# Kernel optimization log

Measured on AMD Instinct MI355X. Metric: run time of the kernel, lower is better.

Reference implementation:

```python
import jax, jax.numpy as jnp
import numpy as np

B, N1, N2, D = 32, 1024, 1024, 128
OUT = 64            # fc1 output / pooled width
SCALE = 0.5         # (input_size // output_size) ** -0.5 = 4 ** -0.5
EPS = 1e-12         # torch F.normalize eps


def _l2norm(x):
    n = jnp.linalg.norm(x, axis=-1, keepdims=True)
    return x / jnp.maximum(n, EPS)


def setup_inputs() -> dict:
    key = jax.random.key(0)
    k1, k2, k3, k4 = jax.random.split(key, 4)
    drug_1 = jax.random.normal(k1, (B, N1, D), dtype=jnp.float32)
    drug_2 = jax.random.normal(k2, (B, N2, D), dtype=jnp.float32)
    # fc1: Linear(256 -> 64), torch default init ~ U(-1/sqrt(256), 1/sqrt(256))
    bound = 1.0 / np.sqrt(2 * D)
    fc1_w = jax.random.uniform(k3, (OUT, 2 * D), jnp.float32, -bound, bound)
    fc1_b = jax.random.uniform(k4, (OUT,), jnp.float32, -bound, bound)
    return {"drug_1": drug_1, "drug_2": drug_2, "fc1_w": fc1_w, "fc1_b": fc1_b}


def reference(drug_1, drug_2, fc1_w, fc1_b):
    d1 = _l2norm(drug_1)                                   # [B,N1,D]
    d2 = _l2norm(drug_2)                                   # [B,N2,D]
    aff = jnp.einsum("bnd,bmd->bnm", d1, d2) * SCALE       # [B,N1,N2]
    s1 = jax.nn.softmax(aff, axis=-1)                      # softmax over N2
    s2 = jax.nn.softmax(aff, axis=-2)                      # softmax over N1
    drug1_layer = jnp.einsum("bnm,bnd->bmd", s2, d1)       # [B,N2,D]
    drug2_layer = jnp.einsum("bnm,bmd->bnd", s1, d2)       # [B,N1,D]
    drug1_emb = jnp.concatenate([d1, drug2_layer], axis=-1)   # [B,N1,2D]
    drug2_emb = jnp.concatenate([d2, drug1_layer], axis=-1)   # [B,N2,2D]
    fusion = jnp.concatenate([drug1_emb, drug2_emb], axis=1)  # [B,N1+N2,2D]
    # dropout treated as identity (deterministic reference)
    w = jax.nn.relu(jnp.einsum("bnf,of->bno", fusion, fc1_w) + fc1_b)
    w = jax.nn.softmax(w, axis=-1)                          # [B,N1+N2,OUT]
    pooled = fusion.reshape(fusion.shape[:-1] + (OUT, 4)).mean(-1)  # AvgPool1d(4)
    return pooled * w
```

## Files before the change

### kernel.cpp

```cpp
#include <hip/hip_runtime.h>

#define Bz   32
#define Nn   1024
#define Dd   128
#define OUTW 64
#define CEXP 0.72134752044448169f
#define LOG2E 1.4426950408889634f

typedef __attribute__((ext_vector_type(8))) short bf16x8;
typedef __attribute__((ext_vector_type(4))) short bf16x4;
typedef __attribute__((ext_vector_type(4))) float f32x4;

static __device__ __forceinline__ unsigned short f2bf(float x) {
    unsigned u = __float_as_uint(x);
    u += 0x7FFFu + ((u >> 16) & 1u);
    return (unsigned short)(u >> 16);
}
static __device__ __forceinline__ float bf2f(short b) {
    return __uint_as_float(((unsigned)(unsigned short)b) << 16);
}
static __device__ __forceinline__ unsigned cvt_pk_bf16(float lo, float hi) {
    unsigned r;
    asm("v_cvt_pk_bf16_f32 %0, %1, %2" : "=v"(r) : "v"(lo), "v"(hi));
    return r;
}
#define GLL16(g, l) __builtin_amdgcn_global_load_lds( \
    (const __attribute__((address_space(1))) unsigned*)(const void*)(g), \
    (__attribute__((address_space(3))) unsigned*)(void*)(l), 16, 0, 0)
#define WAITVN(n) { asm volatile("s_waitcnt vmcnt(" #n ")" ::: "memory"); \
                    __builtin_amdgcn_sched_barrier(0); }
#define SBAR() __builtin_amdgcn_s_barrier()


__global__ __launch_bounds__(256) void k_norm(const float* __restrict__ drug1,
                                              const float* __restrict__ drug2,
                                              short* __restrict__ d1s,
                                              short* __restrict__ d2s,
                                              short* __restrict__ d1ts,
                                              short* __restrict__ d2ts) {
    __shared__ __attribute__((aligned(16))) short T[Dd * 64];
    const int tid = threadIdx.x, wave = tid >> 6, lane = tid & 63;
    const int b = blockIdx.y;
    const int n0 = blockIdx.x * 64;
    const float* src; short* dstR; short* dstT;
    if (blockIdx.z == 0) { src = drug1; dstR = d1s; dstT = d1ts; }
    else                 { src = drug2; dstR = d2s; dstT = d2ts; }

    const int rh = lane >> 5;
    const int c  = lane & 31;
    #pragma unroll
    for (int i = 0; i < 8; ++i) {
        const int col = wave * 16 + i * 2 + rh;
        const int n = n0 + col;
        const float4 v = *(const float4*)(src + ((long)b * Nn + n) * Dd + c * 4);
        float ss = v.x * v.x + v.y * v.y + v.z * v.z + v.w * v.w;
        #pragma unroll
        for (int msk = 1; msk < 32; msk <<= 1) ss += __shfl_xor(ss, msk, 64);
        const float inv = 1.0f / fmaxf(sqrtf(ss), 1e-12f);
        const unsigned p0 = cvt_pk_bf16(v.x * inv, v.y * inv);
        const unsigned p1 = cvt_pk_bf16(v.z * inv, v.w * inv);
        uint2 u2; u2.x = p0; u2.y = p1;
        *(uint2*)(dstR + ((long)b * Nn + n) * Dd + ((c * 4) ^ ((n & 7) * 8))) = u2;
        const unsigned short e0 = (unsigned short)(p0 & 0xFFFF);
        const unsigned short e1 = (unsigned short)(p0 >> 16);
        const unsigned short e2 = (unsigned short)(p1 & 0xFFFF);
        const unsigned short e3 = (unsigned short)(p1 >> 16);
        const int Csw = (16 * (c >> 3)) ^ (8 * (c & 3));
        const int pc = col ^ Csw;
        T[(c * 4 + 0) * 64 + pc] = (short)e0;
        T[(c * 4 + 1) * 64 + pc] = (short)e1;
        T[(c * 4 + 2) * 64 + pc] = (short)e2;
        T[(c * 4 + 3) * 64 + pc] = (short)e3;
    }
    __syncthreads();
    const int d = tid >> 1, h = tid & 1;
    const int C = (16 * (d >> 5)) ^ (8 * ((d >> 2) & 3));
    short* wtp = dstT + ((long)b * Dd + d) * Nn + n0;
    #pragma unroll
    for (int k = 0; k < 4; ++k) {
        const int gi = h * 4 + k;
        *(bf16x8*)(wtp + ((gi ^ (d & 7)) * 8)) =
            *(const bf16x8*)&T[d * 64 + ((gi * 8) ^ C)];
    }
}

__global__ __launch_bounds__(256, 2) void k_attn(const short* __restrict__ d1s,
                                                 const short* __restrict__ d2s,
                                                 const short* __restrict__ d1ts,
                                                 const short* __restrict__ d2ts,
                                                 short* __restrict__ layerA,
                                                 short* __restrict__ layerB) {
    __shared__ __attribute__((aligned(16))) short Kl[2][64][128];
    __shared__ __attribute__((aligned(16))) short Vl[2][128][64];

    const int bid = blockIdx.x;
    const int xcd = bid & 7, tt = bid >> 3;
    const int jq = tt & 7, gq = tt >> 3;
    const int grp = xcd + 8 * gq;
    const int b = grp & 31, z = grp >> 5;

    const int tid = threadIdx.x, wave = tid >> 6, lane = tid & 63;
    const int m = lane & 15, g = lane >> 4;
    const short *Q, *Ks, *Vts; short* O;
    if (z == 0) { Q = d1s; Ks = d2s; Vts = d2ts; O = layerA; }
    else        { Q = d2s; Ks = d1s; Vts = d1ts; O = layerB; }
    const int q0 = jq * 128 + wave * 32;
    const int sw = (m & 7) * 8;

    const short* Qb = Q + ((long)b * Nn + q0) * Dd;
    bf16x8 qf[2][4];
    #pragma unroll
    for (int qt = 0; qt < 2; ++qt)
        #pragma unroll
        for (int c = 0; c < 4; ++c)
            qf[qt][c] = *(const bf16x8*)(Qb + (qt * 16 + m) * Dd
                                            + ((c * 32 + g * 8) ^ sw));

    f32x4 oacc[2][8];
    f32x4 acc_l[2];
    #pragma unroll
    for (int qt = 0; qt < 2; ++qt) {
        acc_l[qt] = (f32x4){0.f, 0.f, 0.f, 0.f};
        #pragma unroll
        for (int t = 0; t < 8; ++t) oacc[qt][t] = (f32x4){0.f, 0.f, 0.f, 0.f};
    }
    bf16x8 ones;
    #pragma unroll
    for (int j = 0; j < 8; ++j) ones[j] = (short)0x3F80;

    const short* Ksb = Ks  + (long)b * Nn * Dd;
    const short* Vtb = Vts + (long)b * Dd * Nn;
    const int klr = lane >> 4, klc = lane & 15;
    const int vlr = lane >> 3, vlc = lane & 7;
    const int srcA = m + 32 * (g & 1);
    const bool glo = (g < 2);

    auto STAGE = [&](int buf, int tile) {
        const int kv0 = tile * 64;
        #pragma unroll
        for (int j = 0; j < 4; ++j)
            GLL16(Ksb + ((long)(kv0 + wave * 16 + j * 4 + klr)) * Dd + klc * 8,
                  &Kl[buf][wave * 16 + j * 4][0]);
        #pragma unroll
        for (int j = 0; j < 4; ++j)
            GLL16(Vtb + ((long)(wave * 32 + j * 8 + vlr)) * Nn + kv0 + vlc * 8,
                  &Vl[buf][wave * 32 + j * 8][0]);
    };

    auto HALF = [&](int buf, int kvsub) {
        f32x4 st[2][2];
        #pragma unroll
        for (int qt = 0; qt < 2; ++qt)
            #pragma unroll
            for (int kt = 0; kt < 2; ++kt) st[qt][kt] = (f32x4){0.f, 0.f, 0.f, 0.f};
        __builtin_amdgcn_s_setprio(1);
        #pragma unroll
        for (int kt = 0; kt < 2; ++kt)
            #pragma unroll
            for (int c = 0; c < 4; ++c) {
                const bf16x8 kf = *(const bf16x8*)
                    &Kl[buf][kvsub + kt * 16 + m][(c * 32 + g * 8) ^ sw];
                st[0][kt] = __builtin_amdgcn_mfma_f32_16x16x32_bf16(kf, qf[0][c], st[0][kt], 0, 0, 0);
                st[1][kt] = __builtin_amdgcn_mfma_f32_16x16x32_bf16(kf, qf[1][c], st[1][kt], 0, 0, 0);
            }
        __builtin_amdgcn_s_setprio(0);
        bf16x8 vf[8];
        #pragma unroll
        for (int t = 0; t < 8; ++t)
            vf[t] = *(const bf16x8*)&Vl[buf][t * 16 + m][(kvsub + g * 8) ^ sw];
        #pragma unroll
        for (int qt = 0; qt < 2; ++qt) {
            unsigned pk[2][2];
            #pragma unroll
            for (int kt = 0; kt < 2; ++kt) {
                const float e0 = exp2f(st[qt][kt][0] * CEXP);
                const float e1 = exp2f(st[qt][kt][1] * CEXP);
                const float e2 = exp2f(st[qt][kt][2] * CEXP);
                const float e3 = exp2f(st[qt][kt][3] * CEXP);
                pk[kt][0] = cvt_pk_bf16(e0, e1);
                pk[kt][1] = cvt_pk_bf16(e2, e3);
            }
            const unsigned w0 = __shfl(pk[0][0], srcA, 64);
            const unsigned w1 = __shfl(pk[0][1], srcA, 64);
            const unsigned w2 = __shfl(pk[0][0], srcA + 16, 64);
            const unsigned w3 = __shfl(pk[0][1], srcA + 16, 64);
            const unsigned x0 = __shfl(pk[1][0], srcA, 64);
            const unsigned x1 = __shfl(pk[1][1], srcA, 64);
            const unsigned x2 = __shfl(pk[1][0], srcA + 16, 64);
            const unsigned x3 = __shfl(pk[1][1], srcA + 16, 64);
            union { unsigned u[4]; bf16x8 v; } af;
            af.u[0] = glo ? w0 : x0;
            af.u[1] = glo ? w1 : x1;
            af.u[2] = glo ? w2 : x2;
            af.u[3] = glo ? w3 : x3;
            __builtin_amdgcn_s_setprio(1);
            #pragma unroll
            for (int t = 0; t < 8; ++t)
                oacc[qt][t] = __builtin_amdgcn_mfma_f32_16x16x32_bf16(af.v, vf[t], oacc[qt][t], 0, 0, 0);
            acc_l[qt] = __builtin_amdgcn_mfma_f32_16x16x32_bf16(af.v, ones, acc_l[qt], 0, 0, 0);
            __builtin_amdgcn_s_setprio(0);
        }
    };

    STAGE(0, 0);
    int cur = 0;
    for (int t = 0; t < 16; ++t) {
        if (t < 15) {
            STAGE(cur ^ 1, t + 1);
            WAITVN(8);
        } else {
            WAITVN(0);
        }
        SBAR();
        HALF(cur, 0);
        HALF(cur, 32);
        asm volatile("s_waitcnt lgkmcnt(0)" ::: "memory");
        SBAR();
        cur ^= 1;
    }

    short* ob = O + ((long)b * Nn + q0) * Dd;
    #pragma unroll
    for (int qt = 0; qt < 2; ++qt)
        #pragma unroll
        for (int r = 0; r < 4; ++r) {
            const float inv = 1.0f / acc_l[qt][r];
            #pragma unroll
            for (int t = 0; t < 8; ++t)
                ob[(qt * 16 + 4 * g + r) * Dd + t * 16 + m] =
                    (short)f2bf(oacc[qt][t][r] * inv);
        }
}

__global__ __launch_bounds__(256, 2) void k_fuse(const float* __restrict__ drug1,
                                                 const float* __restrict__ drug2,
                                                 const short* __restrict__ d1s,
                                                 const short* __restrict__ d2s,
                                                 const short* __restrict__ layA,
                                                 const short* __restrict__ layB,
                                                 const float* __restrict__ fc1w,
                                                 const float* __restrict__ fc1b,
                                                 float* __restrict__ out) {
    const int tid = threadIdx.x, wave = tid >> 6, lane = tid & 63;
    const int m = lane & 15, g = lane >> 4;

    bf16x8 wb[4][8];
    #pragma unroll
    for (int t = 0; t < 4; ++t)
        #pragma unroll
        for (int c = 0; c < 8; ++c) {
            const float* wp = fc1w + (t * 16 + m) * 256 + c * 32 + g * 8;
            const float4 a = *(const float4*)wp;
            const float4 bq = *(const float4*)(wp + 4);
            union { unsigned u[4]; bf16x8 v; } pk;
            pk.u[0] = cvt_pk_bf16(a.x, a.y);
            pk.u[1] = cvt_pk_bf16(a.z, a.w);
            pk.u[2] = cvt_pk_bf16(bq.x, bq.y);
            pk.u[3] = cvt_pk_bf16(bq.z, bq.w);
            wb[t][c] = pk.v;
        }
    float bias[4];
    #pragma unroll
    for (int t = 0; t < 4; ++t) bias[t] = fc1b[t * 16 + m];

    #pragma unroll
    for (int cc = 0; cc < 2; ++cc) {
        const int row0 = blockIdx.x * 128 + cc * 64 + wave * 16;
        const int bb = row0 >> 11;
        const int i0 = row0 & 2047;
        const bool hf = (i0 >= Nn);
        const int ii = hf ? i0 - Nn : i0;
        const short* dsrc = (hf ? d2s : d1s) + ((long)bb * Nn + ii) * Dd;
        const short* lsrc = (hf ? layB : layA) + ((long)bb * Nn + ii) * Dd;
        const float* fsrc = (hf ? drug2 : drug1) + ((long)bb * Nn + ii) * Dd;

        f32x4 acc[4];
        #pragma unroll
        for (int t = 0; t < 4; ++t) acc[t] = (f32x4){0.f, 0.f, 0.f, 0.f};
        #pragma unroll
        for (int c = 0; c < 8; ++c) {
            const short* ap = (c < 4)
                ? dsrc + (long)m * Dd + ((c * 32 + g * 8) ^ ((m & 7) * 8))
                : lsrc + (long)m * Dd + (c - 4) * 32 + g * 8;
            const bf16x8 af = *(const bf16x8*)ap;
            #pragma unroll
            for (int t = 0; t < 4; ++t)
                acc[t] = __builtin_amdgcn_mfma_f32_16x16x32_bf16(af, wb[t][c], acc[t], 0, 0, 0);
        }
        #pragma unroll
        for (int r = 0; r < 4; ++r) {
            float v[4];
            #pragma unroll
            for (int t = 0; t < 4; ++t) v[t] = fmaxf(acc[t][r] + bias[t], 0.f);
            float mx = fmaxf(fmaxf(v[0], v[1]), fmaxf(v[2], v[3]));
            #pragma unroll
            for (int msk = 1; msk < 16; msk <<= 1)
                mx = fmaxf(mx, __shfl_xor(mx, msk, 64));
            float e[4], sum = 0.f;
            #pragma unroll
            for (int t = 0; t < 4; ++t) { e[t] = exp2f((v[t] - mx) * LOG2E); sum += e[t]; }
            #pragma unroll
            for (int msk = 1; msk < 16; msk <<= 1) sum += __shfl_xor(sum, msk, 64);
            const float rinv = 1.0f / sum;

            const int rr = 4 * g + r;
            const float* fr = fsrc + (long)rr * Dd;
            const short* lr = lsrc + (long)rr * Dd;
            const float4 d0 = *(const float4*)(fr + 4 * m);
            const float4 d1 = *(const float4*)(fr + 64 + 4 * m);
            float ss = d0.x*d0.x + d0.y*d0.y + d0.z*d0.z + d0.w*d0.w
                     + d1.x*d1.x + d1.y*d1.y + d1.z*d1.z + d1.w*d1.w;
            #pragma unroll
            for (int msk = 1; msk < 16; msk <<= 1) ss += __shfl_xor(ss, msk, 64);
            const float ninv = 1.0f / fmaxf(sqrtf(ss), 1e-12f);
            const short4 l0 = *(const short4*)(lr + 4 * m);
            const short4 l1 = *(const short4*)(lr + 64 + 4 * m);
            float pooled[4];
            pooled[0] = 0.25f * (d0.x + d0.y + d0.z + d0.w) * ninv;
            pooled[1] = 0.25f * (d1.x + d1.y + d1.z + d1.w) * ninv;
            pooled[2] = 0.25f * (bf2f(l0.x) + bf2f(l0.y) + bf2f(l0.z) + bf2f(l0.w));
            pooled[3] = 0.25f * (bf2f(l1.x) + bf2f(l1.y) + bf2f(l1.z) + bf2f(l1.w));
            float* op = out + ((long)row0 + rr) * OUTW;
            #pragma unroll
            for (int t = 0; t < 4; ++t) op[t * 16 + m] = pooled[t] * (e[t] * rinv);
        }
    }
}

extern "C" void kernel_launch(void* const* d_in, const int* in_sizes, int n_in,
                              void* d_out, int out_size, void* d_ws, size_t ws_size,
                              hipStream_t stream) {
    const float* drug1 = (const float*)d_in[0];
    const float* drug2 = (const float*)d_in[1];
    const float* fc1w  = (const float*)d_in[2];
    const float* fc1b  = (const float*)d_in[3];
    float* out = (float*)d_out;

    char* ws = (char*)d_ws;
    short* d1s    = (short*)(ws);
    short* d2s    = (short*)(ws + 8388608);
    short* d1ts   = (short*)(ws + 16777216);
    short* d2ts   = (short*)(ws + 25165824);
    short* layerA = (short*)(ws + 33554432);
    short* layerB = (short*)(ws + 41943040);

    hipLaunchKernelGGL(k_norm, dim3(16, 32, 2), dim3(256), 0, stream,
                       drug1, drug2, d1s, d2s, d1ts, d2ts);
    hipLaunchKernelGGL(k_attn, dim3(512), dim3(256), 0, stream,
                       d1s, d2s, d1ts, d2ts, layerA, layerB);
    hipLaunchKernelGGL(k_fuse, dim3(512), dim3(256), 0, stream,
                       drug1, drug2, d1s, d2s, layerA, layerB, fc1w, fc1b, out);
}
```

Before: 168.1 us.

## Switch attention to 32x32x16 MFMA with permlane swap and scalar row sums

Rewrites the attention inner loop to use 32x32x16 bf16 MFMA tiles instead of 16x16x32. It builds the P operand in registers with v_permlane32_swap in place of eight cross-lane shuffles, and replaces the ones-vector MFMA row-sum with a plain register accumulation. The fuse kernel also stops rereading the fp32 inputs and recomputing norms, and pools from the already normalized bf16 copies instead. The goal is fewer MFMA and shuffle instructions and less global traffic, at the cost of bf16 precision in the pooled branch and different register pressure.

```diff
diff --git a/kernel.cpp b/kernel.cpp
--- a/kernel.cpp
+++ b/kernel.cpp
@@ -10,6 +10,7 @@
 typedef __attribute__((ext_vector_type(8))) short bf16x8;
 typedef __attribute__((ext_vector_type(4))) short bf16x4;
 typedef __attribute__((ext_vector_type(4))) float f32x4;
+typedef __attribute__((ext_vector_type(16))) float f32x16;
 
 static __device__ __forceinline__ unsigned short f2bf(float x) {
     unsigned u = __float_as_uint(x);
@@ -24,6 +25,8 @@
     asm("v_cvt_pk_bf16_f32 %0, %1, %2" : "=v"(r) : "v"(lo), "v"(hi));
     return r;
 }
+#define PLSWAP(a, b) asm("v_permlane32_swap_b32 %0, %1" : "+v"(a), "+v"(b))
+
 #define GLL16(g, l) __builtin_amdgcn_global_load_lds( \
     (const __attribute__((address_space(1))) unsigned*)(const void*)(g), \
     (__attribute__((address_space(3))) unsigned*)(void*)(l), 16, 0, 0)
@@ -100,40 +103,29 @@
     const int b = grp & 31, z = grp >> 5;
 
     const int tid = threadIdx.x, wave = tid >> 6, lane = tid & 63;
-    const int m = lane & 15, g = lane >> 4;
+    const int r31 = lane & 31, h8 = lane >> 5, r7 = lane & 7;
     const short *Q, *Ks, *Vts; short* O;
     if (z == 0) { Q = d1s; Ks = d2s; Vts = d2ts; O = layerA; }
     else        { Q = d2s; Ks = d1s; Vts = d1ts; O = layerB; }
     const int q0 = jq * 128 + wave * 32;
-    const int sw = (m & 7) * 8;
 
     const short* Qb = Q + ((long)b * Nn + q0) * Dd;
-    bf16x8 qf[2][4];
-    #pragma unroll
-    for (int qt = 0; qt < 2; ++qt)
-        #pragma unroll
-        for (int c = 0; c < 4; ++c)
-            qf[qt][c] = *(const bf16x8*)(Qb + (qt * 16 + m) * Dd
-                                            + ((c * 32 + g * 8) ^ sw));
-
-    f32x4 oacc[2][8];
-    f32x4 acc_l[2];
-    #pragma unroll
-    for (int qt = 0; qt < 2; ++qt) {
-        acc_l[qt] = (f32x4){0.f, 0.f, 0.f, 0.f};
-        #pragma unroll
-        for (int t = 0; t < 8; ++t) oacc[qt][t] = (f32x4){0.f, 0.f, 0.f, 0.f};
-    }
-    bf16x8 ones;
-    #pragma unroll
-    for (int j = 0; j < 8; ++j) ones[j] = (short)0x3F80;
+    bf16x8 qf[8];
+    #pragma unroll
+    for (int c = 0; c < 8; ++c)
+        qf[c] = *(const bf16x8*)(Qb + (long)r31 * Dd + (((2 * c + h8) ^ r7) * 8));
+
+    f32x16 oacc[4];
+    #pragma unroll
+    for (int dblk = 0; dblk < 4; ++dblk)
+        #pragma unroll
+        for (int r = 0; r < 16; ++r) oacc[dblk][r] = 0.f;
+    float lsum = 0.f;
 
     const short* Ksb = Ks  + (long)b * Nn * Dd;
     const short* Vtb = Vts + (long)b * Dd * Nn;
     const int klr = lane >> 4, klc = lane & 15;
     const int vlr = lane >> 3, vlc = lane & 7;
-    const int srcA = m + 32 * (g & 1);
-    const bool glo = (g < 2);
 
     auto STAGE = [&](int buf, int tile) {
         const int kv0 = tile * 64;
@@ -147,59 +139,50 @@
                   &Vl[buf][wave * 32 + j * 8][0]);
     };
 
-    auto HALF = [&](int buf, int kvsub) {
-        f32x4 st[2][2];
-        #pragma unroll
-        for (int qt = 0; qt < 2; ++qt)
-            #pragma unroll
-            for (int kt = 0; kt < 2; ++kt) st[qt][kt] = (f32x4){0.f, 0.f, 0.f, 0.f};
+    auto SUB = [&](int buf, int sub) {
+        f32x16 st;
+        #pragma unroll
+        for (int r = 0; r < 16; ++r) st[r] = 0.f;
         __builtin_amdgcn_s_setprio(1);
         #pragma unroll
-        for (int kt = 0; kt < 2; ++kt)
-            #pragma unroll
-            for (int c = 0; c < 4; ++c) {
-                const bf16x8 kf = *(const bf16x8*)
-                    &Kl[buf][kvsub + kt * 16 + m][(c * 32 + g * 8) ^ sw];
-                st[0][kt] = __builtin_amdgcn_mfma_f32_16x16x32_bf16(kf, qf[0][c], st[0][kt], 0, 0, 0);
-                st[1][kt] = __builtin_amdgcn_mfma_f32_16x16x32_bf16(kf, qf[1][c], st[1][kt], 0, 0, 0);
-            }
+        for (int c = 0; c < 8; ++c) {
+            const bf16x8 kf = *(const bf16x8*)
+                &Kl[buf][sub * 32 + r31][((2 * c + h8) ^ r7) * 8];
+            st = __builtin_amdgcn_mfma_f32_32x32x16_bf16(kf, qf[c], st, 0, 0, 0);
+        }
         __builtin_amdgcn_s_setprio(0);
-        bf16x8 vf[8];
-        #pragma unroll
-        for (int t = 0; t < 8; ++t)
-            vf[t] = *(const bf16x8*)&Vl[buf][t * 16 + m][(kvsub + g * 8) ^ sw];
-        #pragma unroll
-        for (int qt = 0; qt < 2; ++qt) {
-            unsigned pk[2][2];
-            #pragma unroll
-            for (int kt = 0; kt < 2; ++kt) {
-                const float e0 = exp2f(st[qt][kt][0] * CEXP);
-                const float e1 = exp2f(st[qt][kt][1] * CEXP);
-                const float e2 = exp2f(st[qt][kt][2] * CEXP);
-                const float e3 = exp2f(st[qt][kt][3] * CEXP);
-                pk[kt][0] = cvt_pk_bf16(e0, e1);
-                pk[kt][1] = cvt_pk_bf16(e2, e3);
-            }
-            const unsigned w0 = __shfl(pk[0][0], srcA, 64);
-            const unsigned w1 = __shfl(pk[0][1], srcA, 64);
-            const unsigned w2 = __shfl(pk[0][0], srcA + 16, 64);
-            const unsigned w3 = __shfl(pk[0][1], srcA + 16, 64);
-            const unsigned x0 = __shfl(pk[1][0], srcA, 64);
-            const unsigned x1 = __shfl(pk[1][1], srcA, 64);
-            const unsigned x2 = __shfl(pk[1][0], srcA + 16, 64);
-            const unsigned x3 = __shfl(pk[1][1], srcA + 16, 64);
-            union { unsigned u[4]; bf16x8 v; } af;
-            af.u[0] = glo ? w0 : x0;
-            af.u[1] = glo ? w1 : x1;
-            af.u[2] = glo ? w2 : x2;
-            af.u[3] = glo ? w3 : x3;
-            __builtin_amdgcn_s_setprio(1);
-            #pragma unroll
-            for (int t = 0; t < 8; ++t)
-                oacc[qt][t] = __builtin_amdgcn_mfma_f32_16x16x32_bf16(af.v, vf[t], oacc[qt][t], 0, 0, 0);
-            acc_l[qt] = __builtin_amdgcn_mfma_f32_16x16x32_bf16(af.v, ones, acc_l[qt], 0, 0, 0);
-            __builtin_amdgcn_s_setprio(0);
-        }
+        bf16x8 vf[2][4];
+        #pragma unroll
+        for (int kvh = 0; kvh < 2; ++kvh)
+            #pragma unroll
+            for (int dblk = 0; dblk < 4; ++dblk)
+                vf[kvh][dblk] = *(const bf16x8*)
+                    &Vl[buf][dblk * 32 + r31][((4 * sub + 2 * kvh + h8) ^ r7) * 8];
+        float p[16];
+        #pragma unroll
+        for (int r = 0; r < 16; ++r) p[r] = exp2f(st[r] * CEXP);
+        float s4[4];
+        #pragma unroll
+        for (int k = 0; k < 4; ++k)
+            s4[k] = (p[4 * k] + p[4 * k + 1]) + (p[4 * k + 2] + p[4 * k + 3]);
+        lsum += (s4[0] + s4[1]) + (s4[2] + s4[3]);
+        unsigned u0 = cvt_pk_bf16(p[0], p[1]),  u1 = cvt_pk_bf16(p[2], p[3]);
+        unsigned u2 = cvt_pk_bf16(p[4], p[5]),  u3 = cvt_pk_bf16(p[6], p[7]);
+        unsigned u4 = cvt_pk_bf16(p[8], p[9]),  u5 = cvt_pk_bf16(p[10], p[11]);
+        unsigned u6 = cvt_pk_bf16(p[12], p[13]), u7 = cvt_pk_bf16(p[14], p[15]);
+        PLSWAP(u0, u2); PLSWAP(u1, u3);
+        PLSWAP(u4, u6); PLSWAP(u5, u7);
+        union { unsigned u[4]; bf16x8 v; } f0, f1;
+        f0.u[0] = u0; f0.u[1] = u1; f0.u[2] = u2; f0.u[3] = u3;
+        f1.u[0] = u4; f1.u[1] = u5; f1.u[2] = u6; f1.u[3] = u7;
+        __builtin_amdgcn_s_setprio(1);
+        #pragma unroll
+        for (int dblk = 0; dblk < 4; ++dblk)
+            oacc[dblk] = __builtin_amdgcn_mfma_f32_32x32x16_bf16(f0.v, vf[0][dblk], oacc[dblk], 0, 0, 0);
+        #pragma unroll
+        for (int dblk = 0; dblk < 4; ++dblk)
+            oacc[dblk] = __builtin_amdgcn_mfma_f32_32x32x16_bf16(f1.v, vf[1][dblk], oacc[dblk], 0, 0, 0);
+        __builtin_amdgcn_s_setprio(0);
     };
 
     STAGE(0, 0);
@@ -212,29 +195,27 @@
             WAITVN(0);
         }
         SBAR();
-        HALF(cur, 0);
-        HALF(cur, 32);
+        SUB(cur, 0);
+        SUB(cur, 1);
         asm volatile("s_waitcnt lgkmcnt(0)" ::: "memory");
         SBAR();
         cur ^= 1;
     }
 
+    const float tot = lsum + __shfl_xor(lsum, 32, 64);
+    const float rinv = 1.0f / tot;
     short* ob = O + ((long)b * Nn + q0) * Dd;
     #pragma unroll
-    for (int qt = 0; qt < 2; ++qt)
-        #pragma unroll
-        for (int r = 0; r < 4; ++r) {
-            const float inv = 1.0f / acc_l[qt][r];
-            #pragma unroll
-            for (int t = 0; t < 8; ++t)
-                ob[(qt * 16 + 4 * g + r) * Dd + t * 16 + m] =
-                    (short)f2bf(oacc[qt][t][r] * inv);
-        }
-}
-
-__global__ __launch_bounds__(256, 2) void k_fuse(const float* __restrict__ drug1,
-                                                 const float* __restrict__ drug2,
-                                                 const short* __restrict__ d1s,
+    for (int r = 0; r < 16; ++r) {
+        const int qq = (r & 3) + 8 * (r >> 2) + 4 * h8;
+        const float inv = __shfl(rinv, qq, 64);
+        #pragma unroll
+        for (int dblk = 0; dblk < 4; ++dblk)
+            ob[qq * Dd + dblk * 32 + r31] = (short)f2bf(oacc[dblk][r] * inv);
+    }
+}
+
+__global__ __launch_bounds__(256, 2) void k_fuse(const short* __restrict__ d1s,
                                                  const short* __restrict__ d2s,
                                                  const short* __restrict__ layA,
                                                  const short* __restrict__ layB,
@@ -272,7 +253,6 @@
         const int ii = hf ? i0 - Nn : i0;
         const short* dsrc = (hf ? d2s : d1s) + ((long)bb * Nn + ii) * Dd;
         const short* lsrc = (hf ? layB : layA) + ((long)bb * Nn + ii) * Dd;
-        const float* fsrc = (hf ? drug2 : drug1) + ((long)bb * Nn + ii) * Dd;
 
         f32x4 acc[4];
         #pragma unroll
@@ -304,22 +284,21 @@
             const float rinv = 1.0f / sum;
 
             const int rr = 4 * g + r;
-            const float* fr = fsrc + (long)rr * Dd;
+            const short* dr = dsrc + (long)rr * Dd;
             const short* lr = lsrc + (long)rr * Dd;
-            const float4 d0 = *(const float4*)(fr + 4 * m);
-            const float4 d1 = *(const float4*)(fr + 64 + 4 * m);
-            float ss = d0.x*d0.x + d0.y*d0.y + d0.z*d0.z + d0.w*d0.w
-                     + d1.x*d1.x + d1.y*d1.y + d1.z*d1.z + d1.w*d1.w;
-            #pragma unroll
-            for (int msk = 1; msk < 16; msk <<= 1) ss += __shfl_xor(ss, msk, 64);
-            const float ninv = 1.0f / fmaxf(sqrtf(ss), 1e-12f);
-            const short4 l0 = *(const short4*)(lr + 4 * m);
-            const short4 l1 = *(const short4*)(lr + 64 + 4 * m);
             float pooled[4];
-            pooled[0] = 0.25f * (d0.x + d0.y + d0.z + d0.w) * ninv;
-            pooled[1] = 0.25f * (d1.x + d1.y + d1.z + d1.w) * ninv;
-            pooled[2] = 0.25f * (bf2f(l0.x) + bf2f(l0.y) + bf2f(l0.z) + bf2f(l0.w));
-            pooled[3] = 0.25f * (bf2f(l1.x) + bf2f(l1.y) + bf2f(l1.z) + bf2f(l1.w));
+            #pragma unroll
+            for (int t = 0; t < 2; ++t) {
+                const int e0 = t * 64 + 4 * m;
+                const int phys = (((e0 >> 3) ^ (rr & 7)) * 8) + (e0 & 7);
+                const short4 s4 = *(const short4*)(dr + phys);
+                pooled[t] = 0.25f * (bf2f(s4.x) + bf2f(s4.y) + bf2f(s4.z) + bf2f(s4.w));
+            }
+            #pragma unroll
+            for (int t = 2; t < 4; ++t) {
+                const short4 s4 = *(const short4*)(lr + (t - 2) * 64 + 4 * m);
+                pooled[t] = 0.25f * (bf2f(s4.x) + bf2f(s4.y) + bf2f(s4.z) + bf2f(s4.w));
+            }
             float* op = out + ((long)row0 + rr) * OUTW;
             #pragma unroll
             for (int t = 0; t < 4; ++t) op[t * 16 + m] = pooled[t] * (e[t] * rinv);
@@ -349,5 +328,5 @@
     hipLaunchKernelGGL(k_attn, dim3(512), dim3(256), 0, stream,
                        d1s, d2s, d1ts, d2ts, layerA, layerB);
     hipLaunchKernelGGL(k_fuse, dim3(512), dim3(256), 0, stream,
-                       drug1, drug2, d1s, d2s, layerA, layerB, fc1w, fc1b, out);
-}
+                       d1s, d2s, layerA, layerB, fc1w, fc1b, out);
+}
```

Result: faster. 158.5 us (-5.8%).
